# Kernel tuning notes

Hardware: AMD Instinct MI355X
Metric: run time of the kernel (lower is better)

Reference implementation:

```python
import jax, jax.numpy as jnp
import numpy as np

B, N, D, H = 4, 2048, 256, 4
DH = D // H          # 64
SCALE = DH ** (-0.5)
LN_EPS = 1e-5


def setup_inputs() -> dict:
    key = jax.random.key(0)
    ks = jax.random.split(key, 16)
    g = lambda k, shape, fan_in: jax.random.normal(k, shape, jnp.float32) / np.sqrt(fan_in)
    # Weights stored as [in, out] (pre-transposed vs torch Linear)
    return {
        "x0": jax.random.normal(ks[0], (B, N, D), jnp.float32),
        "x1": jax.random.normal(ks[1], (B, N, D), jnp.float32),
        "Wqk": g(ks[2], (D, D), D), "bqk": jnp.zeros((D,), jnp.float32),
        "Wv": g(ks[3], (D, D), D), "bv": jnp.zeros((D,), jnp.float32),
        "Wout": g(ks[4], (D, D), D), "bout": jnp.zeros((D,), jnp.float32),
        "Wf1": g(ks[5], (2 * D, 2 * D), 2 * D), "bf1": jnp.zeros((2 * D,), jnp.float32),
        "ln_g": jnp.ones((2 * D,), jnp.float32), "ln_b": jnp.zeros((2 * D,), jnp.float32),
        "Wf2": g(ks[6], (2 * D, D), 2 * D), "bf2": jnp.zeros((D,), jnp.float32),
    }


def _split_heads(t):
    # [B,N,D] -> [B,H,N,DH]
    b, n, _ = t.shape
    return t.reshape(b, n, H, DH).transpose(0, 2, 1, 3)


def _merge_heads(t):
    # [B,H,N,DH] -> [B,N,D]
    b, h, n, dh = t.shape
    return t.transpose(0, 2, 1, 3).reshape(b, n, h * dh)


def _layernorm(x, g, b):
    mu = jnp.mean(x, axis=-1, keepdims=True)
    var = jnp.mean(jnp.square(x - mu), axis=-1, keepdims=True)
    return (x - mu) * jax.lax.rsqrt(var + LN_EPS) * g + b


def reference(x0, x1, Wqk, bqk, Wv, bv, Wout, bout, Wf1, bf1, ln_g, ln_b, Wf2, bf2):
    qk0 = _split_heads(x0 @ Wqk + bqk)   # [B,H,N,DH]
    qk1 = _split_heads(x1 @ Wqk + bqk)
    v0 = _split_heads(x0 @ Wv + bv)
    v1 = _split_heads(x1 @ Wv + bv)

    ss = SCALE ** 0.5
    sim = jnp.einsum('bhid,bhjd->bhij', qk0 * ss, qk1 * ss)  # shared score matrix
    attn01 = jax.nn.softmax(sim, axis=-1)   # normalize over j
    attn10 = jax.nn.softmax(sim, axis=-2)   # normalize over i (== softmax(sim^T) transposed)
    m0 = jnp.einsum('bhij,bhjd->bhid', attn01, v1)
    m1 = jnp.einsum('bhji,bhjd->bhid', attn10, v0)

    m0 = _merge_heads(m0) @ Wout + bout   # [B,N,D]
    m1 = _merge_heads(m1) @ Wout + bout

    def ffn(x):
        h = x @ Wf1 + bf1                 # [B,N,2D]
        h = jax.nn.gelu(_layernorm(h, ln_g, ln_b), approximate=False)
        return h @ Wf2 + bf2              # [B,N,D]

    y0 = x0 + ffn(jnp.concatenate([x0, m0], axis=-1))
    y1 = x1 + ffn(jnp.concatenate([x1, m1], axis=-1))
    return (y0, y1)
```

## Files before the change

### kernel.cpp

```cpp
#include <hip/hip_runtime.h>
#include <hip/hip_bf16.h>
#include <math.h>

typedef __bf16 bf16;
typedef __attribute__((ext_vector_type(8))) __bf16 bf16x8;
typedef __attribute__((ext_vector_type(4))) __bf16 bf16x4;
typedef __attribute__((ext_vector_type(2))) __bf16 bf16x2;
typedef __attribute__((ext_vector_type(4))) float f32x4;
typedef __attribute__((ext_vector_type(16))) float f32x16;
typedef __attribute__((ext_vector_type(4))) unsigned u32x4;

#define MFMA(a,b,c)   __builtin_amdgcn_mfma_f32_16x16x32_bf16(a,b,c,0,0,0)
#define MFMA32(a,b,c) __builtin_amdgcn_mfma_f32_32x32x16_bf16(a,b,c,0,0,0)

static constexpr int Bb = 4, Nn = 2048, Hh = 4;
static constexpr float SS2 = 0.4246609001440095f;

__device__ __forceinline__ void lds16(const bf16* src, bf16* dst) {
  __builtin_amdgcn_global_load_lds(
      (const __attribute__((address_space(1))) void*)src,
      (__attribute__((address_space(3))) void*)dst, 16, 0, 0);
}

__device__ __forceinline__ f32x16 zero16() {
  f32x16 t;
#pragma unroll
  for (int i = 0; i < 16; ++i) t[i] = 0.f;
  return t;
}

__global__ __launch_bounds__(256) void prep_k(
    const float* Wqk, const float* Wv, const float* Wout, const float* bout,
    const float* Wf1, const float* Wf2, const float* x0, const float* x1,
    bf16* wqkv_t, bf16* wout_b, bf16* wfold_t, bf16* wf1b_t, bf16* wf2_t,
    bf16* xb0, bf16* xb1) {
  int id = blockIdx.x * 256 + threadIdx.x;
  if (id < 65536) { int k = id >> 8, n = id & 255; wqkv_t[n*256 + k] = (bf16)Wqk[id]; return; }
  id -= 65536;
  if (id < 65536) { int k = id >> 8, n = id & 255; wqkv_t[(256 + n)*256 + k] = (bf16)Wv[id]; return; }
  id -= 65536;
  if (id < 98304) {
    if (id < 65536) { wout_b[id] = (bf16)Wout[id]; }
    else { int id3 = id - 65536; int r = id3 >> 8, k = id3 & 255;
           wout_b[(256 + r)*256 + k] = (r == 0) ? (bf16)bout[k] : (bf16)0.f; }
    return; }
  id -= 98304;
  if (id < 131072) { int o = id & 511, k = id >> 9; wfold_t[o*512 + k] = (bf16)Wf1[k*512 + o]; return; }
  id -= 131072;
  if (id < 131072) { int o = id & 511, k = id >> 9; wf1b_t[o*256 + k] = (bf16)Wf1[(256 + k)*512 + o]; return; }
  id -= 131072;
  if (id < 131072) { int k = id >> 8, n = id & 255; wf2_t[n*512 + k] = (bf16)Wf2[id]; return; }
  id -= 131072;
  if (id < 1048576) {
    const float* xs = (id < 524288) ? x0 : x1;
    bf16* xd = (id < 524288) ? xb0 : xb1;
    int j = (id < 524288) ? id : id - 524288;
    f32x4 v = *reinterpret_cast<const f32x4*>(&xs[(size_t)j * 4]);
    bf16x4 o; o[0] = (bf16)v[0]; o[1] = (bf16)v[1]; o[2] = (bf16)v[2]; o[3] = (bf16)v[3];
    *reinterpret_cast<bf16x4*>(&xd[(size_t)j * 4]) = o;
  }
}

template<int MODE, int BN, int MINW>
__global__ __launch_bounds__(256, MINW) void gemm_k(
    const bf16* Aa0, const bf16* Aa1, const bf16* Ac0, const bf16* Ac1,
    const bf16* Wt, const float* bias,
    bf16* ob0, bf16* ob1, float* of0, float* of1,
    const float* res0, const float* res1) {
  constexpr int KD  = (MODE == 3 || MODE == 4) ? 512 : 256;
  constexpr int LDA = (MODE == 4) ? 512 : 256;
  constexpr int NKC = KD / 64;
  constexpr int NF  = BN / 32;

  const int z = blockIdx.z;
  const bf16* Aa = z ? Aa1 : Aa0;
  const bf16* Ac = z ? Ac1 : Ac0;
  bf16*  ob = z ? ob1 : ob0;
  float* of = z ? of1 : of0;
  const float* res = z ? res1 : res0;

  const int tid = threadIdx.x;
  const int lane = tid & 63;
  const int w = tid >> 6;
  const int wr = w >> 1, wc = w & 1;
  const int m0r = blockIdx.x * 128;
  const int n0 = blockIdx.y * BN;
  const int r15 = lane & 15, g = lane >> 4, rb = r15 & 7;
  const int l3 = lane >> 3, l7 = lane & 7;
  const int swzc = (l7 ^ l3) * 8;

  __shared__ bf16 At[2][8192];
  __shared__ bf16 Bt[2][BN * 64];

  const bf16* aA = Aa + (size_t)(m0r + w*32 + l3) * LDA + swzc;
  const bf16* aC = (MODE == 3) ? (Ac + (size_t)(m0r + w*32 + l3) * 256 + swzc) : nullptr;
  const bf16* bB = Wt + (size_t)(n0 + w*(BN/4) + l3) * KD + swzc;
  const int adst = (w*32) * 64;
  const int bdst = (w*(BN/4)) * 64;

  auto stage = [&](int buf, int kc) {
    const bf16* ab; int kcol;
    if constexpr (MODE == 3) {
      if (kc < 4) { ab = aA; kcol = kc * 64; } else { ab = aC; kcol = (kc - 4) * 64; }
    } else { ab = aA; kcol = kc * 64; }
#pragma unroll
    for (int i = 0; i < 4; i++)
      lds16(ab + kcol + (size_t)i * 8 * LDA, &At[buf][adst + i*512]);
#pragma unroll
    for (int i = 0; i < NF; i++)
      lds16(bB + kc*64 + (size_t)i * 8 * KD, &Bt[buf][bdst + i*512]);
  };

  f32x4 acc[4][NF];
#pragma unroll
  for (int i = 0; i < 4; i++)
#pragma unroll
    for (int j = 0; j < NF; j++) acc[i][j] = f32x4{0.f, 0.f, 0.f, 0.f};

  const int rx0 = ((0*4 + g) ^ rb) << 4;
  const int rx1 = ((1*4 + g) ^ rb) << 4;

  auto compute = [&](int cur) {
    const char* Ap = (const char*)&At[cur][0];
    const char* Bp = (const char*)&Bt[cur][0];
    __builtin_amdgcn_s_setprio(1);
#pragma unroll
    for (int ks = 0; ks < 2; ++ks) {
      const int rx = ks ? rx1 : rx0;
      bf16x8 af[4], bfr[NF];
#pragma unroll
      for (int mf = 0; mf < 4; ++mf)
        af[mf] = *reinterpret_cast<const bf16x8*>(Ap + (wr*64 + mf*16 + r15) * 128 + rx);
#pragma unroll
      for (int nf = 0; nf < NF; ++nf)
        bfr[nf] = *reinterpret_cast<const bf16x8*>(Bp + (wc*(BN/2) + nf*16 + r15) * 128 + rx);
#pragma unroll
      for (int mf = 0; mf < 4; ++mf)
#pragma unroll
        for (int nf = 0; nf < NF; ++nf)
          acc[mf][nf] = MFMA(af[mf], bfr[nf], acc[mf][nf]);
    }
    __builtin_amdgcn_s_setprio(0);
  };

  stage(0, 0);
  int cur = 0;
  for (int kc = 0; kc < NKC - 1; ++kc) {
    stage(cur ^ 1, kc + 1);
    if constexpr (NF == 4) asm volatile("s_waitcnt vmcnt(8)" ::: "memory");
    else                   asm volatile("s_waitcnt vmcnt(6)" ::: "memory");
    __builtin_amdgcn_sched_barrier(0);
    __builtin_amdgcn_s_barrier();
    __builtin_amdgcn_sched_barrier(0);
    compute(cur);
    asm volatile("s_waitcnt lgkmcnt(0)" ::: "memory");
    __builtin_amdgcn_sched_barrier(0);
    __builtin_amdgcn_s_barrier();
    __builtin_amdgcn_sched_barrier(0);
    cur ^= 1;
  }
  asm volatile("s_waitcnt vmcnt(0)" ::: "memory");
  __builtin_amdgcn_sched_barrier(0);
  __builtin_amdgcn_s_barrier();
  __builtin_amdgcn_sched_barrier(0);
  compute(cur);

#pragma unroll
  for (int mf = 0; mf < 4; ++mf)
#pragma unroll
    for (int nf = 0; nf < NF; ++nf) {
      f32x4 c = acc[mf][nf];
      int cg = n0 + wc*(BN/2) + nf*16 + r15;
#pragma unroll
      for (int r = 0; r < 4; ++r) {
        int rg = m0r + wr*64 + mf*16 + g*4 + r;
        if constexpr (MODE == 5) {
          int b = rg >> 11, n = rg & 2047;
          if (cg < 256) {
            float val = (c[r] + bias[cg]) * SS2;
            int h = cg >> 6, dh = cg & 63;
            ob[(((size_t)(b*Hh + h)) * Nn + n) * 64 + dh] = (bf16)val;
          } else {
            int c2 = cg - 256;
            float val = c[r] + res[c2];
            int h = c2 >> 6, dh = c2 & 63;
            ((bf16*)of)[(((size_t)(b*Hh + h)) * 64 + dh) * Nn + n] = (bf16)val;
          }
        } else if constexpr (MODE == 6) {
          if (rg < 256) ob[(size_t)cg * 512 + 256 + rg] = (bf16)c[r];
          else if (rg == 256) of[cg] = c[r] + bias[cg];
        } else if constexpr (MODE == 3) {
          ob[(size_t)rg * 512 + cg] = (bf16)(c[r] + bias[cg]);
        } else {
          of[(size_t)rg * 256 + cg] = c[r] + bias[cg] + (float)Ac[(size_t)rg * 256 + cg];
        }
      }
    }
}

__global__ __launch_bounds__(256, 2) void attn_k(
    const bf16* qks0, const bf16* qks1, const bf16* vT0, const bf16* vT1,
    bf16* m0o, bf16* m1o) {
  const int B = blockIdx.x + 16 * (blockIdx.y + 16 * blockIdx.z);
  const int xcd = B & 7, kk = B >> 3;
  const int group = 4 * xcd + (kk >> 4);
  const int it = kk & 15;
  const int bh = group & 15, dir = group >> 4;

  const bf16* Q  = (dir ? qks1 : qks0) + (size_t)bh * (Nn * 64);
  const bf16* Kp = (dir ? qks0 : qks1) + (size_t)bh * (Nn * 64);
  const bf16* Vp = (dir ? vT0  : vT1 ) + (size_t)bh * (64 * Nn);
  bf16* out = dir ? m1o : m0o;
  const int b = bh >> 2, h = bh & 3;

  const int tid = threadIdx.x, lane = tid & 63, w = tid >> 6;
  const int l31 = lane & 31, hi = lane >> 5, xr = l31 & 7;
  const int iw = it * 128 + w * 32;

  __shared__ bf16 Kt[4][4096];
  __shared__ bf16 Vt[4][4096];
  __shared__ float Rt[4][32];

  bf16x8 qf[4];
#pragma unroll
  for (int kt = 0; kt < 4; ++kt)
    qf[kt] = *reinterpret_cast<const bf16x8*>(
        &Q[(size_t)(iw + l31) * 64 + kt*16 + hi*8]);

  f32x16 acc[2]; acc[0] = zero16(); acc[1] = zero16();
  float rsum = 0.f;

  const int l3 = lane >> 3, l7 = lane & 7;
  const int swz = ((l7 ^ l3) * 8);
  const bf16* ks0 = Kp + (size_t)(w*16 +     l3) * 64 + swz;
  const bf16* ks1 = Kp + (size_t)(w*16 + 8 + l3) * 64 + swz;
  const bf16* vs0 = Vp + (size_t)(w*16 +     l3) * 2048 + swz;
  const bf16* vs1 = Vp + (size_t)(w*16 + 8 + l3) * 2048 + swz;
  const int kd0 = (w*16    ) * 64;
  const int kd1 = (w*16 + 8) * 64;

  auto stage = [&](int buf, int j0) {
    lds16(ks0 + (size_t)j0 * 64, &Kt[buf][kd0]);
    lds16(ks1 + (size_t)j0 * 64, &Kt[buf][kd1]);
    lds16(vs0 + j0,              &Vt[buf][kd0]);
    lds16(vs1 + j0,              &Vt[buf][kd1]);
  };

  int kby[2][4], vby[2][4];
#pragma unroll
  for (int jm = 0; jm < 2; ++jm)
#pragma unroll
    for (int kt = 0; kt < 4; ++kt)
      kby[jm][kt] = (jm*32 + l31) * 128 + (((2*kt + hi) ^ xr) << 4);
#pragma unroll
  for (int nt = 0; nt < 2; ++nt)
#pragma unroll
    for (int gg = 0; gg < 4; ++gg)
      vby[nt][gg] = (nt*32 + l31) * 128 + (((2*gg + hi) ^ xr) << 4);

  auto compute_tile = [&](int cur) {
    const char* Kb = (const char*)&Kt[cur][0];
    const char* Vb = (const char*)&Vt[cur][0];
    f32x16 st[2];
    __builtin_amdgcn_s_setprio(1);
#pragma unroll
    for (int jm = 0; jm < 2; ++jm) {
      f32x16 t = zero16();
#pragma unroll
      for (int kt = 0; kt < 4; ++kt) {
        bf16x8 kf = *reinterpret_cast<const bf16x8*>(Kb + kby[jm][kt]);
        t = MFMA32(kf, qf[kt], t);
      }
      st[jm] = t;
    }
    __builtin_amdgcn_s_setprio(0);
    bf16x8 pa[4];
#pragma unroll
    for (int jm = 0; jm < 2; ++jm) {
      unsigned dw[8];
#pragma unroll
      for (int s = 0; s < 8; ++s) {
        float e0 = __builtin_amdgcn_exp2f(st[jm][2*s]);
        float e1 = __builtin_amdgcn_exp2f(st[jm][2*s + 1]);
        rsum += e0 + e1;
        bf16x2 p; p[0] = (bf16)e0; p[1] = (bf16)e1;
        dw[s] = __builtin_bit_cast(unsigned, p);
      }
#pragma unroll
      for (int kt2 = 0; kt2 < 2; ++kt2) {
        unsigned a0 = dw[4*kt2 + 0], b0 = dw[4*kt2 + 2];
        unsigned a1 = dw[4*kt2 + 1], b1 = dw[4*kt2 + 3];
        asm volatile("v_permlane32_swap_b32 %0, %1" : "+v"(a0), "+v"(b0));
        asm volatile("v_permlane32_swap_b32 %0, %1" : "+v"(a1), "+v"(b1));
        u32x4 uu; uu[0] = a0; uu[1] = a1; uu[2] = b0; uu[3] = b1;
        pa[jm*2 + kt2] = __builtin_bit_cast(bf16x8, uu);
      }
    }
    __builtin_amdgcn_s_setprio(1);
#pragma unroll
    for (int gg = 0; gg < 4; ++gg) {
#pragma unroll
      for (int nt = 0; nt < 2; ++nt) {
        bf16x8 vf = *reinterpret_cast<const bf16x8*>(Vb + vby[nt][gg]);
        acc[nt] = MFMA32(pa[gg], vf, acc[nt]);
      }
    }
    __builtin_amdgcn_s_setprio(0);
  };

  stage(0, 0); stage(1, 1 << 6); stage(2, 2 << 6);
  for (int jt = 0; jt < 30; ++jt) {
    asm volatile("s_waitcnt vmcnt(8)" ::: "memory");
    __builtin_amdgcn_sched_barrier(0);
    __builtin_amdgcn_s_barrier();
    __builtin_amdgcn_sched_barrier(0);
    stage((jt + 3) & 3, (jt + 3) << 6);
    compute_tile(jt & 3);
  }
  asm volatile("s_waitcnt vmcnt(4)" ::: "memory");
  __builtin_amdgcn_sched_barrier(0);
  __builtin_amdgcn_s_barrier();
  __builtin_amdgcn_sched_barrier(0);
  compute_tile(2);
  asm volatile("s_waitcnt vmcnt(0)" ::: "memory");
  __builtin_amdgcn_sched_barrier(0);
  __builtin_amdgcn_s_barrier();
  __builtin_amdgcn_sched_barrier(0);
  compute_tile(3);

  rsum += __shfl_xor(rsum, 32);
  if (lane < 32) Rt[w][l31] = rsum;
  f32x4 rv[4];
#pragma unroll
  for (int q = 0; q < 4; ++q)
    rv[q] = *reinterpret_cast<const f32x4*>(&Rt[w][8*q + 4*hi]);
#pragma unroll
  for (int r = 0; r < 16; ++r) {
    float inv = 1.0f / rv[r >> 2][r & 3];
    int row = iw + (r & 3) + 8*(r >> 2) + 4*hi;
#pragma unroll
    for (int nt = 0; nt < 2; ++nt) {
      int col = h*64 + nt*32 + l31;
      out[((size_t)b * Nn + row) * 256 + col] = (bf16)(acc[nt][r] * inv);
    }
  }
}

__global__ __launch_bounds__(256) void ln_gelu_k(
    bf16* hg, const float* g, const float* bb) {
  const int row = (blockIdx.x << 2) + (threadIdx.x >> 6);
  const int lane = threadIdx.x & 63;
  bf16* hr = hg + (size_t)row * 512 + lane * 8;
  bf16x8 v = *reinterpret_cast<const bf16x8*>(hr);
  float f[8];
  float s = 0.f, sq = 0.f;
#pragma unroll
  for (int i = 0; i < 8; ++i) { f[i] = (float)v[i]; s += f[i]; sq += f[i]*f[i]; }
#pragma unroll
  for (int m = 1; m < 64; m <<= 1) { s += __shfl_xor(s, m); sq += __shfl_xor(sq, m); }
  float mu = s * (1.f / 512.f);
  float var = sq * (1.f / 512.f) - mu * mu;
  float rsv = rsqrtf(var + 1e-5f);
  f32x4 g0 = *reinterpret_cast<const f32x4*>(&g[lane*8]);
  f32x4 g1 = *reinterpret_cast<const f32x4*>(&g[lane*8 + 4]);
  f32x4 b0 = *reinterpret_cast<const f32x4*>(&bb[lane*8]);
  f32x4 b1 = *reinterpret_cast<const f32x4*>(&bb[lane*8 + 4]);
  bf16x8 o;
#pragma unroll
  for (int i = 0; i < 8; ++i) {
    float gv = (i < 4) ? g0[i] : g1[i-4];
    float bv = (i < 4) ? b0[i] : b1[i-4];
    float xn = (f[i] - mu) * rsv * gv + bv;
    float ge = 0.5f * xn * (1.f + erff(xn * 0.70710678118f));
    o[i] = (bf16)ge;
  }
  *reinterpret_cast<bf16x8*>(hr) = o;
}

extern "C" void kernel_launch(void* const* d_in, const int* in_sizes, int n_in,
                              void* d_out, int out_size, void* d_ws, size_t ws_size,
                              hipStream_t stream) {
  (void)in_sizes; (void)n_in; (void)out_size; (void)ws_size;
  const float* x0   = (const float*)d_in[0];
  const float* x1   = (const float*)d_in[1];
  const float* Wqk  = (const float*)d_in[2];
  const float* bqk  = (const float*)d_in[3];
  const float* Wv   = (const float*)d_in[4];
  const float* bv   = (const float*)d_in[5];
  const float* Wout = (const float*)d_in[6];
  const float* bout = (const float*)d_in[7];
  const float* Wf1  = (const float*)d_in[8];
  const float* bf1  = (const float*)d_in[9];
  const float* ln_g = (const float*)d_in[10];
  const float* ln_b = (const float*)d_in[11];
  const float* Wf2  = (const float*)d_in[12];
  const float* bf2  = (const float*)d_in[13];
  float* y = (float*)d_out;

  bf16* p = (bf16*)d_ws;
  bf16* wqkv_t = p; p += 131072;
  bf16* wout_b = p; p += 98304;
  bf16* wfold_t = p; p += 262144;
  bf16* wf1b_t = p; p += 131072;
  bf16* wf2_t  = p; p += 131072;
  float* bfold = (float*)p; p += 1024;
  bf16* xb0  = p; p += 2097152;
  bf16* xb1  = p; p += 2097152;
  bf16* qks0 = p; p += 2097152;
  bf16* qks1 = p; p += 2097152;
  bf16* vT0  = p; p += 2097152;
  bf16* vT1  = p; p += 2097152;
  bf16* m0   = p; p += 2097152;
  bf16* m1   = p; p += 2097152;
  bf16* hg0  = p; p += 4194304;
  bf16* hg1  = p; p += 4194304;

  dim3 blk(256);
  prep_k<<<6528, blk, 0, stream>>>(Wqk, Wv, Wout, bout, Wf1, Wf2, x0, x1,
                                   wqkv_t, wout_b, wfold_t, wf1b_t, wf2_t, xb0, xb1);
  gemm_k<6,128,2><<<dim3(3, 4, 1), blk, 0, stream>>>(
      wout_b, wout_b, nullptr, nullptr, wf1b_t, bf1,
      wfold_t, wfold_t, bfold, bfold, nullptr, nullptr);
  gemm_k<5,128,2><<<dim3(64, 4, 2), blk, 0, stream>>>(
      xb0, xb1, nullptr, nullptr, wqkv_t, bqk,
      qks0, qks1, (float*)vT0, (float*)vT1, bv, bv);
  attn_k<<<dim3(16, 16, 2), blk, 0, stream>>>(qks0, qks1, vT0, vT1, m0, m1);
  gemm_k<3,128,2><<<dim3(64, 4, 2), blk, 0, stream>>>(
      xb0, xb1, m0, m1, wfold_t, bfold,
      hg0, hg1, nullptr, nullptr, nullptr, nullptr);
  ln_gelu_k<<<dim3(4096), blk, 0, stream>>>(hg0, ln_g, ln_b);
  gemm_k<4,64,3><<<dim3(64, 4, 2), blk, 0, stream>>>(
      hg0, hg1, xb0, xb1, wf2_t, bf2,
      nullptr, nullptr, y, y + 2097152, nullptr, nullptr);
}
```

Baseline: 130.4 us.

## Remap GEMM blocks per XCD, MFMA row sums, double-buffer attention K/V

GEMM block indices are remapped so consecutive hardware block IDs land on adjacent M tiles per XCD, aiming for better L2 reuse of the weight and activation tiles. In attention, the softmax row sums are now computed by an extra MFMA against a vector of ones instead of scalar adds, a shuffle and an LDS reduction. Packed bf16 conversion uses inline asm. The K/V pipeline shrinks from four buffers to two, with an extra barrier per tile, trading prefetch depth for lower LDS use and possibly higher occupancy. The row sums are now taken from bf16-rounded probabilities rather than fp32 values.

```diff
diff --git a/kernel.cpp b/kernel.cpp
--- a/kernel.cpp
+++ b/kernel.cpp
@@ -61,7 +61,7 @@
   }
 }
 
-template<int MODE, int BN, int MINW>
+template<int MODE, int BN, int MINW, int REMAP>
 __global__ __launch_bounds__(256, MINW) void gemm_k(
     const bf16* Aa0, const bf16* Aa1, const bf16* Ac0, const bf16* Ac1,
     const bf16* Wt, const float* bias,
@@ -72,19 +72,26 @@
   constexpr int NKC = KD / 64;
   constexpr int NF  = BN / 32;
 
-  const int z = blockIdx.z;
-  const bf16* Aa = z ? Aa1 : Aa0;
-  const bf16* Ac = z ? Ac1 : Ac0;
-  bf16*  ob = z ? ob1 : ob0;
-  float* of = z ? of1 : of0;
-  const float* res = z ? res1 : res0;
+  int bx = blockIdx.x, by = blockIdx.y, bz = blockIdx.z;
+  if constexpr (REMAP) {
+    int id = blockIdx.x + 64 * (blockIdx.y + 4 * blockIdx.z);
+    bx = ((id & 7) << 3) + ((id >> 3) & 7);
+    by = (id >> 6) & 3;
+    bz = id >> 8;
+  }
+
+  const bf16* Aa = bz ? Aa1 : Aa0;
+  const bf16* Ac = bz ? Ac1 : Ac0;
+  bf16*  ob = bz ? ob1 : ob0;
+  float* of = bz ? of1 : of0;
+  const float* res = bz ? res1 : res0;
 
   const int tid = threadIdx.x;
   const int lane = tid & 63;
   const int w = tid >> 6;
   const int wr = w >> 1, wc = w & 1;
-  const int m0r = blockIdx.x * 128;
-  const int n0 = blockIdx.y * BN;
+  const int m0r = bx * 128;
+  const int n0 = by * BN;
   const int r15 = lane & 15, g = lane >> 4, rb = r15 & 7;
   const int l3 = lane >> 3, l7 = lane & 7;
   const int swzc = (l7 ^ l3) * 8;
@@ -217,9 +224,8 @@
   const int l31 = lane & 31, hi = lane >> 5, xr = l31 & 7;
   const int iw = it * 128 + w * 32;
 
-  __shared__ bf16 Kt[4][4096];
-  __shared__ bf16 Vt[4][4096];
-  __shared__ float Rt[4][32];
+  __shared__ bf16 Kt[2][4096];
+  __shared__ bf16 Vt[2][4096];
 
   bf16x8 qf[4];
 #pragma unroll
@@ -227,8 +233,12 @@
     qf[kt] = *reinterpret_cast<const bf16x8*>(
         &Q[(size_t)(iw + l31) * 64 + kt*16 + hi*8]);
 
+  bf16x8 ones;
+#pragma unroll
+  for (int i = 0; i < 8; ++i) ones[i] = (bf16)1.0f;
+
   f32x16 acc[2]; acc[0] = zero16(); acc[1] = zero16();
-  float rsum = 0.f;
+  f32x16 rsacc = zero16();
 
   const int l3 = lane >> 3, l7 = lane & 7;
   const int swz = ((l7 ^ l3) * 8);
@@ -282,9 +292,7 @@
       for (int s = 0; s < 8; ++s) {
         float e0 = __builtin_amdgcn_exp2f(st[jm][2*s]);
         float e1 = __builtin_amdgcn_exp2f(st[jm][2*s + 1]);
-        rsum += e0 + e1;
-        bf16x2 p; p[0] = (bf16)e0; p[1] = (bf16)e1;
-        dw[s] = __builtin_bit_cast(unsigned, p);
+        asm("v_cvt_pk_bf16_f32 %0, %1, %2" : "=v"(dw[s]) : "v"(e0), "v"(e1));
       }
 #pragma unroll
       for (int kt2 = 0; kt2 < 2; ++kt2) {
@@ -299,6 +307,7 @@
     __builtin_amdgcn_s_setprio(1);
 #pragma unroll
     for (int gg = 0; gg < 4; ++gg) {
+      rsacc = MFMA32(pa[gg], ones, rsacc);
 #pragma unroll
       for (int nt = 0; nt < 2; ++nt) {
         bf16x8 vf = *reinterpret_cast<const bf16x8*>(Vb + vby[nt][gg]);
@@ -308,35 +317,30 @@
     __builtin_amdgcn_s_setprio(0);
   };
 
-  stage(0, 0); stage(1, 1 << 6); stage(2, 2 << 6);
-  for (int jt = 0; jt < 30; ++jt) {
-    asm volatile("s_waitcnt vmcnt(8)" ::: "memory");
+  stage(0, 0);
+  int cur = 0;
+  for (int jt = 0; jt < 31; ++jt) {
+    stage(cur ^ 1, (jt + 1) << 6);
+    asm volatile("s_waitcnt vmcnt(4)" ::: "memory");
     __builtin_amdgcn_sched_barrier(0);
     __builtin_amdgcn_s_barrier();
     __builtin_amdgcn_sched_barrier(0);
-    stage((jt + 3) & 3, (jt + 3) << 6);
-    compute_tile(jt & 3);
-  }
-  asm volatile("s_waitcnt vmcnt(4)" ::: "memory");
-  __builtin_amdgcn_sched_barrier(0);
-  __builtin_amdgcn_s_barrier();
-  __builtin_amdgcn_sched_barrier(0);
-  compute_tile(2);
+    compute_tile(cur);
+    asm volatile("s_waitcnt lgkmcnt(0)" ::: "memory");
+    __builtin_amdgcn_sched_barrier(0);
+    __builtin_amdgcn_s_barrier();
+    __builtin_amdgcn_sched_barrier(0);
+    cur ^= 1;
+  }
   asm volatile("s_waitcnt vmcnt(0)" ::: "memory");
   __builtin_amdgcn_sched_barrier(0);
   __builtin_amdgcn_s_barrier();
   __builtin_amdgcn_sched_barrier(0);
-  compute_tile(3);
-
-  rsum += __shfl_xor(rsum, 32);
-  if (lane < 32) Rt[w][l31] = rsum;
-  f32x4 rv[4];
-#pragma unroll
-  for (int q = 0; q < 4; ++q)
-    rv[q] = *reinterpret_cast<const f32x4*>(&Rt[w][8*q + 4*hi]);
+  compute_tile(cur);
+
 #pragma unroll
   for (int r = 0; r < 16; ++r) {
-    float inv = 1.0f / rv[r >> 2][r & 3];
+    float inv = 1.0f / rsacc[r];
     int row = iw + (r & 3) + 8*(r >> 2) + 4*hi;
 #pragma unroll
     for (int nt = 0; nt < 2; ++nt) {
@@ -418,18 +422,18 @@
   dim3 blk(256);
   prep_k<<<6528, blk, 0, stream>>>(Wqk, Wv, Wout, bout, Wf1, Wf2, x0, x1,
                                    wqkv_t, wout_b, wfold_t, wf1b_t, wf2_t, xb0, xb1);
-  gemm_k<6,128,2><<<dim3(3, 4, 1), blk, 0, stream>>>(
+  gemm_k<6,128,2,0><<<dim3(3, 4, 1), blk, 0, stream>>>(
       wout_b, wout_b, nullptr, nullptr, wf1b_t, bf1,
       wfold_t, wfold_t, bfold, bfold, nullptr, nullptr);
-  gemm_k<5,128,2><<<dim3(64, 4, 2), blk, 0, stream>>>(
+  gemm_k<5,128,2,1><<<dim3(64, 4, 2), blk, 0, stream>>>(
       xb0, xb1, nullptr, nullptr, wqkv_t, bqk,
       qks0, qks1, (float*)vT0, (float*)vT1, bv, bv);
   attn_k<<<dim3(16, 16, 2), blk, 0, stream>>>(qks0, qks1, vT0, vT1, m0, m1);
-  gemm_k<3,128,2><<<dim3(64, 4, 2), blk, 0, stream>>>(
+  gemm_k<3,128,2,1><<<dim3(64, 4, 2), blk, 0, stream>>>(
       xb0, xb1, m0, m1, wfold_t, bfold,
       hg0, hg1, nullptr, nullptr, nullptr, nullptr);
   ln_gelu_k<<<dim3(4096), blk, 0, stream>>>(hg0, ln_g, ln_b);
-  gemm_k<4,64,3><<<dim3(64, 4, 2), blk, 0, stream>>>(
+  gemm_k<4,64,3,1><<<dim3(64, 4, 2), blk, 0, stream>>>(
       hg0, hg1, xb0, xb1, wf2_t, bf2,
       nullptr, nullptr, y, y + 2097152, nullptr, nullptr);
 }
```

New measurement: 129.8 us. About the same (-0.5%).
